# Optimization experiments

Measured on AMD Instinct MI355X. Metric: run time of the kernel, lower is better.

The kernel has to match this reference:

```python
import jax, jax.numpy as jnp
import numpy as np

B, L, H, NH = 2, 2048, 1024, 16
HD = H // NH  # head dim = 64


def setup_inputs() -> dict:
    key = jax.random.key(0)
    ks = jax.random.split(key, 8)
    s = 0.02  # small init scale for weights
    return {
        "q": jax.random.normal(ks[0], (B, L, H), jnp.float32),
        "k": jax.random.normal(ks[1], (B, L, H), jnp.float32),
        "v": jax.random.normal(ks[2], (B, L, H), jnp.float32),
        "attention_mask": jnp.zeros((B, NH, L, L), jnp.float32),
        "Wq": jax.random.normal(ks[3], (H, H), jnp.float32) * s,
        "bq": jnp.zeros((H,), jnp.float32),
        "Wk": jax.random.normal(ks[4], (H, H), jnp.float32) * s,
        "bk": jnp.zeros((H,), jnp.float32),
        "Wv": jax.random.normal(ks[5], (H, H), jnp.float32) * s,
        "bv": jnp.zeros((H,), jnp.float32),
        "Wo": jax.random.normal(ks[6], (H, H), jnp.float32) * s,
        "bo": jnp.zeros((H,), jnp.float32),
    }


def reference(q, k, v, attention_mask, Wq, bq, Wk, bk, Wv, bv, Wo, bo):
    # Conv1D (GPT-2 style) projections: x @ W + b
    query = q @ Wq + bq  # [B, L, H]
    key = k @ Wk + bk
    value = v @ Wv + bv
    # split heads -> [B, NH, L, HD]
    qh = query.reshape(B, L, NH, HD).transpose(0, 2, 1, 3)
    kh = key.reshape(B, L, NH, HD).transpose(0, 2, 1, 3)
    vh = value.reshape(B, L, NH, HD).transpose(0, 2, 1, 3)
    # scores: [B, NH, L, L]
    w = jnp.einsum("bhqd,bhkd->bhqk", qh, kh) / jnp.sqrt(jnp.float32(HD))
    w = w + attention_mask
    w = jax.nn.softmax(w, axis=-1)  # dropout p=0 -> identity
    out = jnp.einsum("bhqk,bhkd->bhqd", w, vh)  # [B, NH, L, HD]
    # merge heads -> [B, L, H]
    out = out.transpose(0, 2, 1, 3).reshape(B, L, H)
    return out @ Wo + bo
```

## Files before the change

### kernel.cpp

```cpp
#include <hip/hip_runtime.h>

#define NBATCH 2
#define LSEQ   2048
#define NH     16
#define HD     64
#define HDIM   1024
#define MTOK   4096

typedef unsigned short u16;
typedef __attribute__((ext_vector_type(8))) short bf16x8;
typedef __attribute__((ext_vector_type(4))) float f32x4;

__device__ __forceinline__ u16 f2bf(float f) {
  union { float f; unsigned int u; } x; x.f = f;
  return (u16)((x.u + 0x7fffu + ((x.u >> 16) & 1u)) >> 16);
}

__device__ __forceinline__ void gload_lds16(const void* g, void* l) {
  __builtin_amdgcn_global_load_lds(
      (const __attribute__((address_space(1))) unsigned int*)g,
      (__attribute__((address_space(3))) unsigned int*)l, 16, 0, 0);
}

__global__ void cvt3_kernel(const float* __restrict__ q, const float* __restrict__ k,
                            const float* __restrict__ v, u16* __restrict__ xq,
                            u16* __restrict__ xk, u16* __restrict__ xv) {
  const float* in;
  u16* out;
  if (blockIdx.z == 0)      { in = q; out = xq; }
  else if (blockIdx.z == 1) { in = k; out = xk; }
  else                      { in = v; out = xv; }
  int i = blockIdx.x * blockDim.x + threadIdx.x;
  float4 t = ((const float4*)in)[i];
  ushort4 o;
  o.x = f2bf(t.x); o.y = f2bf(t.y); o.z = f2bf(t.z); o.w = f2bf(t.w);
  ((ushort4*)out)[i] = o;
}

__global__ void wt4_kernel(const float* __restrict__ W0, const float* __restrict__ W1,
                           const float* __restrict__ W2, const float* __restrict__ W3,
                           u16* __restrict__ T0, u16* __restrict__ T1,
                           u16* __restrict__ T2, u16* __restrict__ T3) {
  const float* W;
  u16* Wt;
  if (blockIdx.z == 0)      { W = W0; Wt = T0; }
  else if (blockIdx.z == 1) { W = W1; Wt = T1; }
  else if (blockIdx.z == 2) { W = W2; Wt = T2; }
  else                      { W = W3; Wt = T3; }
  __shared__ float tile[64][65];
  const int k0 = (blockIdx.x & 15) << 6;
  const int n0 = (blockIdx.x >> 4) << 6;
  const int t = threadIdx.x;
#pragma unroll
  for (int i = 0; i < 4; ++i) {
    int idx = t + i * 256;
    int r = idx >> 4, c = (idx & 15) << 2;
    float4 v = *(const float4*)&W[(size_t)(k0 + r) * HDIM + n0 + c];
    tile[r][c] = v.x; tile[r][c + 1] = v.y; tile[r][c + 2] = v.z; tile[r][c + 3] = v.w;
  }
  __syncthreads();
#pragma unroll
  for (int i = 0; i < 4; ++i) {
    int idx = t + i * 256;
    int r = idx >> 4, c = (idx & 15) << 2;
    ushort4 o;
    o.x = f2bf(tile[c][r]);     o.y = f2bf(tile[c + 1][r]);
    o.z = f2bf(tile[c + 2][r]); o.w = f2bf(tile[c + 3][r]);
    *(ushort4*)&Wt[(size_t)(n0 + r) * HDIM + k0 + c] = o;
  }
}

template <int MODE>
__device__ __forceinline__ void gemm_core(u16* As, u16* Bs,
    const u16* __restrict__ A, const u16* __restrict__ Bt,
    const float* __restrict__ bias, void* __restrict__ Cout) {
  const int tid = threadIdx.x;
  const int lane = tid & 63, wid = tid >> 6;
  const int l15 = lane & 15, g = lane >> 4;
  const int m0 = blockIdx.y * 128, n0 = blockIdx.x * 128;
  const int wr = wid >> 1, wc = wid & 1;
  f32x4 acc[4][4];
#pragma unroll
  for (int i = 0; i < 4; ++i)
#pragma unroll
    for (int j = 0; j < 4; ++j) acc[i][j] = (f32x4){0.f, 0.f, 0.f, 0.f};

  for (int t = 0; t < HDIM / 64; ++t) {
    const int k0 = t * 64;
    __syncthreads();
#pragma unroll
    for (int i = 0; i < 4; ++i) {
      const int row = wid * 32 + i * 8 + (lane >> 3);
      const int colb = (lane & 7) * 16;
      gload_lds16((const char*)(A + (size_t)(m0 + row) * HDIM + k0) + colb,
                  (char*)As + (wid * 32 + i * 8) * 128);
      gload_lds16((const char*)(Bt + (size_t)(n0 + row) * HDIM + k0) + colb,
                  (char*)Bs + (wid * 32 + i * 8) * 128);
    }
    __syncthreads();
#pragma unroll
    for (int ks = 0; ks < 2; ++ks) {
      bf16x8 a[4], b[4];
#pragma unroll
      for (int i = 0; i < 4; ++i) {
        const int row = wr * 64 + i * 16 + l15;
        a[i] = *(const bf16x8*)((const char*)As + row * 128 + ks * 64 + g * 16);
      }
#pragma unroll
      for (int j = 0; j < 4; ++j) {
        const int row = wc * 64 + j * 16 + l15;
        b[j] = *(const bf16x8*)((const char*)Bs + row * 128 + ks * 64 + g * 16);
      }
#pragma unroll
      for (int i = 0; i < 4; ++i)
#pragma unroll
        for (int j = 0; j < 4; ++j)
          acc[i][j] = __builtin_amdgcn_mfma_f32_16x16x32_bf16(a[i], b[j], acc[i][j], 0, 0, 0);
    }
  }
#pragma unroll
  for (int i = 0; i < 4; ++i) {
    const int mrow = m0 + wr * 64 + i * 16 + 4 * g;
#pragma unroll
    for (int j = 0; j < 4; ++j) {
      const int ncol = n0 + wc * 64 + j * 16 + l15;
      const float bb = bias[ncol];
      if (MODE == 3) {
        float* o = (float*)Cout;
#pragma unroll
        for (int r = 0; r < 4; ++r)
          o[(size_t)(mrow + r) * HDIM + ncol] = acc[i][j][r] + bb;
      } else if (MODE == 2) {
        const int bidx = mrow >> 11, l0 = mrow & (LSEQ - 1);
        const int h = ncol >> 6, d = ncol & 63;
        ushort4 o4;
        o4.x = f2bf(acc[i][j][0] + bb); o4.y = f2bf(acc[i][j][1] + bb);
        o4.z = f2bf(acc[i][j][2] + bb); o4.w = f2bf(acc[i][j][3] + bb);
        *(ushort4*)&((u16*)Cout)[(((size_t)bidx * NH + h) * HD + d) * LSEQ + l0] = o4;
      } else {
        const int h = ncol >> 6, d = ncol & 63;
        u16* o = (u16*)Cout;
#pragma unroll
        for (int r = 0; r < 4; ++r) {
          const int m = mrow + r;
          const int bidx = m >> 11, l = m & (LSEQ - 1);
          o[(((size_t)bidx * NH + h) * LSEQ + l) * HD + d] = f2bf(acc[i][j][r] + bb);
        }
      }
    }
  }
}

__global__ __launch_bounds__(256, 2) void proj_gemm_kernel(
    const u16* __restrict__ xq, const u16* __restrict__ xk, const u16* __restrict__ xv,
    const u16* __restrict__ WqT, const u16* __restrict__ WkT, const u16* __restrict__ WvT,
    const float* __restrict__ bq, const float* __restrict__ bk, const float* __restrict__ bv,
    u16* __restrict__ Qh, u16* __restrict__ Kh, u16* __restrict__ Vt) {
  __shared__ u16 As[128 * 64];
  __shared__ u16 Bs[128 * 64];
  if (blockIdx.z == 0)      gemm_core<0>(As, Bs, xq, WqT, bq, Qh);
  else if (blockIdx.z == 1) gemm_core<0>(As, Bs, xk, WkT, bk, Kh);
  else                      gemm_core<2>(As, Bs, xv, WvT, bv, Vt);
}

__global__ __launch_bounds__(256, 2) void out_gemm_kernel(
    const u16* __restrict__ A, const u16* __restrict__ WoT,
    const float* __restrict__ bo, float* __restrict__ out) {
  __shared__ u16 As[128 * 64];
  __shared__ u16 Bs[128 * 64];
  gemm_core<3>(As, Bs, A, WoT, bo, out);
}

__global__ __launch_bounds__(256, 4) void attn_kernel(
    const u16* __restrict__ Qh, const u16* __restrict__ Kh,
    const u16* __restrict__ Vt, const float* __restrict__ mask,
    u16* __restrict__ Out ) {
  __shared__ u16 Ks[2][64 * 64];
  __shared__ u16 Vs[2][64 * 64];
  __shared__ u16 Ps[4][16 * 64];
  const int lane = threadIdx.x & 63, w = threadIdx.x >> 6;
  const int l15 = lane & 15, g = lane >> 4;
  const int bh = blockIdx.y;
  const int q0 = blockIdx.x * 64 + w * 16;

  bf16x8 aq[2];
  {
    const u16* qbase = Qh + ((size_t)bh * LSEQ + q0 + l15) * HD;
    aq[0] = *(const bf16x8*)(qbase + g * 8);
    aq[1] = *(const bf16x8*)(qbase + 32 + g * 8);
  }
  f32x4 o_acc[4];
#pragma unroll
  for (int db = 0; db < 4; ++db) o_acc[db] = (f32x4){0.f, 0.f, 0.f, 0.f};
  float m_r[4], l_r[4];
#pragma unroll
  for (int r = 0; r < 4; ++r) { m_r[r] = -1e30f; l_r[r] = 0.f; }

  const size_t kbase = (size_t)bh * LSEQ * HD;
  const size_t vbase = (size_t)bh * HD * LSEQ;
  const int srow = w * 16 + (lane >> 3);
  const int scolb = (lane & 7) * 16;

#define STAGE(buf, tt) do {                                                    \
    const int kv0_ = (tt) * 64;                                                \
    _Pragma("unroll")                                                          \
    for (int i_ = 0; i_ < 2; ++i_) {                                           \
      const int row_ = srow + i_ * 8;                                          \
      const int cb_ = scolb ^ ((row_ & 7) << 4);                               \
      gload_lds16((const char*)(Kh + kbase + (size_t)(kv0_ + row_) * HD) + cb_,\
                  (char*)Ks[buf] + (w * 16 + i_ * 8) * 128);                   \
      gload_lds16((const char*)(Vt + vbase + (size_t)row_ * LSEQ + kv0_) + cb_,\
                  (char*)Vs[buf] + (w * 16 + i_ * 8) * 128);                   \
    }                                                                          \
  } while (0)

  STAGE(0, 0);
  __syncthreads();

  int cur = 0;
  const float* mbase0 = mask + ((size_t)bh * LSEQ + q0 + 4 * g) * LSEQ + l15;
  u16* pbase = Ps[w];

  for (int t = 0; t < LSEQ / 64; ++t) {
    const int kv0 = t * 64;
    if (t + 1 < LSEQ / 64) STAGE(cur ^ 1, t + 1);

    float mv[4][4];
#pragma unroll
    for (int r = 0; r < 4; ++r)
#pragma unroll
      for (int nb = 0; nb < 4; ++nb)
        mv[r][nb] = mbase0[(size_t)r * LSEQ + kv0 + nb * 16];

    f32x4 s_acc[4];
#pragma unroll
    for (int nb = 0; nb < 4; ++nb) s_acc[nb] = (f32x4){0.f, 0.f, 0.f, 0.f};
#pragma unroll
    for (int ks = 0; ks < 2; ++ks) {
#pragma unroll
      for (int nb = 0; nb < 4; ++nb) {
        const int row = nb * 16 + l15;
        bf16x8 bk = *(const bf16x8*)((const char*)Ks[cur] + row * 128 +
                                     ((ks * 64 + g * 16) ^ ((row & 7) << 4)));
        s_acc[nb] = __builtin_amdgcn_mfma_f32_16x16x32_bf16(aq[ks], bk, s_acc[nb], 0, 0, 0);
      }
    }

#pragma unroll
    for (int r = 0; r < 4; ++r) {
      float v0 = s_acc[0][r] * 0.125f + mv[r][0];
      float v1 = s_acc[1][r] * 0.125f + mv[r][1];
      float v2 = s_acc[2][r] * 0.125f + mv[r][2];
      float v3 = s_acc[3][r] * 0.125f + mv[r][3];
      float mm = fmaxf(fmaxf(v0, v1), fmaxf(v2, v3));
      mm = fmaxf(mm, __shfl_xor(mm, 1));
      mm = fmaxf(mm, __shfl_xor(mm, 2));
      mm = fmaxf(mm, __shfl_xor(mm, 4));
      mm = fmaxf(mm, __shfl_xor(mm, 8));
      const float mnew = fmaxf(m_r[r], mm);
      const float cf = __expf(m_r[r] - mnew);
      m_r[r] = mnew;
      float p0 = __expf(v0 - mnew), p1 = __expf(v1 - mnew);
      float p2 = __expf(v2 - mnew), p3 = __expf(v3 - mnew);
      float s0 = p0 + p1 + p2 + p3;
      s0 += __shfl_xor(s0, 1); s0 += __shfl_xor(s0, 2);
      s0 += __shfl_xor(s0, 4); s0 += __shfl_xor(s0, 8);
      l_r[r] = l_r[r] * cf + s0;
#pragma unroll
      for (int db = 0; db < 4; ++db) o_acc[db][r] *= cf;
      const int q = 4 * g + r;
      const int qx = (q & 7) << 4;
      *(u16*)((char*)pbase + q * 128 + ((0 + 2 * l15) ^ qx)) = f2bf(p0);
      *(u16*)((char*)pbase + q * 128 + ((32 + 2 * l15) ^ qx)) = f2bf(p1);
      *(u16*)((char*)pbase + q * 128 + ((64 + 2 * l15) ^ qx)) = f2bf(p2);
      *(u16*)((char*)pbase + q * 128 + ((96 + 2 * l15) ^ qx)) = f2bf(p3);
    }
    asm volatile("s_waitcnt lgkmcnt(0)" ::: "memory");
    __builtin_amdgcn_sched_barrier(0);

#pragma unroll
    for (int s = 0; s < 2; ++s) {
      bf16x8 pa = *(const bf16x8*)((const char*)pbase + l15 * 128 +
                                   ((s * 64 + 16 * g) ^ ((l15 & 7) << 4)));
#pragma unroll
      for (int db = 0; db < 4; ++db) {
        const int row = db * 16 + l15;
        bf16x8 bv = *(const bf16x8*)((const char*)Vs[cur] + row * 128 +
                                     ((s * 64 + 16 * g) ^ ((row & 7) << 4)));
        o_acc[db] = __builtin_amdgcn_mfma_f32_16x16x32_bf16(pa, bv, o_acc[db], 0, 0, 0);
      }
    }
    __syncthreads();
    cur ^= 1;
  }
#undef STAGE

  const int b = bh >> 4, h = bh & 15;
#pragma unroll
  for (int r = 0; r < 4; ++r) {
    const float inv = 1.f / l_r[r];
    const int qg = q0 + 4 * g + r;
    u16* orow = Out + ((size_t)(b * LSEQ + qg) * NH + h) * HD;
#pragma unroll
    for (int db = 0; db < 4; ++db)
      orow[db * 16 + l15] = f2bf(o_acc[db][r] * inv);
  }
}

extern "C" void kernel_launch(void* const* d_in, const int* in_sizes, int n_in,
                              void* d_out, int out_size, void* d_ws, size_t ws_size,
                              hipStream_t stream) {
  (void)in_sizes; (void)n_in; (void)out_size; (void)ws_size;
  const float* q    = (const float*)d_in[0];
  const float* k    = (const float*)d_in[1];
  const float* v    = (const float*)d_in[2];
  const float* mask = (const float*)d_in[3];
  const float* Wq   = (const float*)d_in[4];
  const float* bq   = (const float*)d_in[5];
  const float* Wk   = (const float*)d_in[6];
  const float* bk   = (const float*)d_in[7];
  const float* Wv   = (const float*)d_in[8];
  const float* bv   = (const float*)d_in[9];
  const float* Wo   = (const float*)d_in[10];
  const float* bo   = (const float*)d_in[11];
  float* out = (float*)d_out;

  char* ws = (char*)d_ws;
  const size_t XB = (size_t)MTOK * HDIM * 2;
  const size_t WB = (size_t)HDIM * HDIM * 2;
  u16* xq   = (u16*)(ws);
  u16* xk   = (u16*)(ws + XB);
  u16* xv   = (u16*)(ws + 2 * XB);
  u16* WqT  = (u16*)(ws + 3 * XB);
  u16* WkT  = (u16*)(ws + 3 * XB + WB);
  u16* WvT  = (u16*)(ws + 3 * XB + 2 * WB);
  u16* WoT  = (u16*)(ws + 3 * XB + 3 * WB);
  u16* Qh   = (u16*)(ws + 3 * XB + 4 * WB);
  u16* Kh   = (u16*)(ws + 4 * XB + 4 * WB);
  u16* Vt   = (u16*)(ws + 5 * XB + 4 * WB);
  u16* aout = (u16*)(ws + 6 * XB + 4 * WB);

  cvt3_kernel<<<dim3((MTOK * HDIM) / 4 / 256, 1, 3), 256, 0, stream>>>(
      q, k, v, xq, xk, xv);
  wt4_kernel<<<dim3(256, 1, 4), 256, 0, stream>>>(
      Wq, Wk, Wv, Wo, WqT, WkT, WvT, WoT);
  proj_gemm_kernel<<<dim3(HDIM / 128, MTOK / 128, 3), 256, 0, stream>>>(
      xq, xk, xv, WqT, WkT, WvT, bq, bk, bv, Qh, Kh, Vt);
  attn_kernel<<<dim3(LSEQ / 64, NBATCH * NH), 256, 0, stream>>>(Qh, Kh, Vt, mask, aout);
  out_gemm_kernel<<<dim3(HDIM / 128, MTOK / 128), 256, 0, stream>>>(aout, WoT, bo, out);
}
```

Before: 246.2 us.

## Transpose QK^T MFMA so each lane owns one query row for softmax

Swaps the MFMA operands for the score computation so each lane holds four scores from a single query row. Softmax max and sum then reduce across only two cross-lane shuffles instead of four per row, and the running max and sum live in one scalar per lane. Mask values are loaded as float4 and prefetched one tile ahead, P is written to LDS as packed 4-element stores, and s_setprio raises wave priority around the MFMA blocks. The cost is extra shuffles to spread rescale factors and row sums back to the output accumulator layout.

```diff
diff --git a/kernel.cpp b/kernel.cpp
--- a/kernel.cpp
+++ b/kernel.cpp
@@ -182,6 +182,7 @@
   const int l15 = lane & 15, g = lane >> 4;
   const int bh = blockIdx.y;
   const int q0 = blockIdx.x * 64 + w * 16;
+  const int NT = LSEQ / 64;
 
   bf16x8 aq[2];
   {
@@ -192,9 +193,7 @@
   f32x4 o_acc[4];
 #pragma unroll
   for (int db = 0; db < 4; ++db) o_acc[db] = (f32x4){0.f, 0.f, 0.f, 0.f};
-  float m_r[4], l_r[4];
-#pragma unroll
-  for (int r = 0; r < 4; ++r) { m_r[r] = -1e30f; l_r[r] = 0.f; }
+  float m_run = -1e30f, l_run = 0.f;
 
   const size_t kbase = (size_t)bh * LSEQ * HD;
   const size_t vbase = (size_t)bh * HD * LSEQ;
@@ -214,74 +213,96 @@
     }                                                                          \
   } while (0)
 
+  const float* mrow = mask + ((size_t)bh * LSEQ + q0 + l15) * LSEQ;
+  f32x4 mv[4];
+
   STAGE(0, 0);
+#pragma unroll
+  for (int mb = 0; mb < 4; ++mb)
+    mv[mb] = *(const f32x4*)(mrow + mb * 16 + 4 * g);
   __syncthreads();
 
   int cur = 0;
-  const float* mbase0 = mask + ((size_t)bh * LSEQ + q0 + 4 * g) * LSEQ + l15;
   u16* pbase = Ps[w];
-
-  for (int t = 0; t < LSEQ / 64; ++t) {
-    const int kv0 = t * 64;
-    if (t + 1 < LSEQ / 64) STAGE(cur ^ 1, t + 1);
-
-    float mv[4][4];
-#pragma unroll
-    for (int r = 0; r < 4; ++r)
-#pragma unroll
-      for (int nb = 0; nb < 4; ++nb)
-        mv[r][nb] = mbase0[(size_t)r * LSEQ + kv0 + nb * 16];
+  const int srcbase = (lane & 48) | ((lane & 48) >> 2);
+  const int pswz = (l15 & 7) << 4;
+
+  for (int t = 0; t < NT; ++t) {
+    if (t + 1 < NT) STAGE(cur ^ 1, t + 1);
 
     f32x4 s_acc[4];
 #pragma unroll
-    for (int nb = 0; nb < 4; ++nb) s_acc[nb] = (f32x4){0.f, 0.f, 0.f, 0.f};
+    for (int mb = 0; mb < 4; ++mb) s_acc[mb] = (f32x4){0.f, 0.f, 0.f, 0.f};
+    __builtin_amdgcn_s_setprio(1);
 #pragma unroll
     for (int ks = 0; ks < 2; ++ks) {
 #pragma unroll
-      for (int nb = 0; nb < 4; ++nb) {
-        const int row = nb * 16 + l15;
+      for (int mb = 0; mb < 4; ++mb) {
+        const int row = mb * 16 + l15;
         bf16x8 bk = *(const bf16x8*)((const char*)Ks[cur] + row * 128 +
                                      ((ks * 64 + g * 16) ^ ((row & 7) << 4)));
-        s_acc[nb] = __builtin_amdgcn_mfma_f32_16x16x32_bf16(aq[ks], bk, s_acc[nb], 0, 0, 0);
-      }
-    }
-
-#pragma unroll
-    for (int r = 0; r < 4; ++r) {
-      float v0 = s_acc[0][r] * 0.125f + mv[r][0];
-      float v1 = s_acc[1][r] * 0.125f + mv[r][1];
-      float v2 = s_acc[2][r] * 0.125f + mv[r][2];
-      float v3 = s_acc[3][r] * 0.125f + mv[r][3];
-      float mm = fmaxf(fmaxf(v0, v1), fmaxf(v2, v3));
-      mm = fmaxf(mm, __shfl_xor(mm, 1));
-      mm = fmaxf(mm, __shfl_xor(mm, 2));
-      mm = fmaxf(mm, __shfl_xor(mm, 4));
-      mm = fmaxf(mm, __shfl_xor(mm, 8));
-      const float mnew = fmaxf(m_r[r], mm);
-      const float cf = __expf(m_r[r] - mnew);
-      m_r[r] = mnew;
-      float p0 = __expf(v0 - mnew), p1 = __expf(v1 - mnew);
-      float p2 = __expf(v2 - mnew), p3 = __expf(v3 - mnew);
-      float s0 = p0 + p1 + p2 + p3;
-      s0 += __shfl_xor(s0, 1); s0 += __shfl_xor(s0, 2);
-      s0 += __shfl_xor(s0, 4); s0 += __shfl_xor(s0, 8);
-      l_r[r] = l_r[r] * cf + s0;
-#pragma unroll
-      for (int db = 0; db < 4; ++db) o_acc[db][r] *= cf;
-      const int q = 4 * g + r;
-      const int qx = (q & 7) << 4;
-      *(u16*)((char*)pbase + q * 128 + ((0 + 2 * l15) ^ qx)) = f2bf(p0);
-      *(u16*)((char*)pbase + q * 128 + ((32 + 2 * l15) ^ qx)) = f2bf(p1);
-      *(u16*)((char*)pbase + q * 128 + ((64 + 2 * l15) ^ qx)) = f2bf(p2);
-      *(u16*)((char*)pbase + q * 128 + ((96 + 2 * l15) ^ qx)) = f2bf(p3);
-    }
+        s_acc[mb] = __builtin_amdgcn_mfma_f32_16x16x32_bf16(bk, aq[ks], s_acc[mb], 0, 0, 0);
+      }
+    }
+    __builtin_amdgcn_s_setprio(0);
+
+    float p[4][4];
+    float tmax = -1e30f;
+#pragma unroll
+    for (int mb = 0; mb < 4; ++mb)
+#pragma unroll
+      for (int r = 0; r < 4; ++r) {
+        p[mb][r] = s_acc[mb][r] * 0.125f + mv[mb][r];
+        tmax = fmaxf(tmax, p[mb][r]);
+      }
+    tmax = fmaxf(tmax, __shfl_xor(tmax, 16));
+    tmax = fmaxf(tmax, __shfl_xor(tmax, 32));
+    const float mnew = fmaxf(m_run, tmax);
+    const float cf = __expf(m_run - mnew);
+    m_run = mnew;
+    float psum = 0.f;
+#pragma unroll
+    for (int mb = 0; mb < 4; ++mb)
+#pragma unroll
+      for (int r = 0; r < 4; ++r) {
+        p[mb][r] = __expf(p[mb][r] - mnew);
+        psum += p[mb][r];
+      }
+    psum += __shfl_xor(psum, 16);
+    psum += __shfl_xor(psum, 32);
+    l_run = l_run * cf + psum;
+    float cfr[4];
+#pragma unroll
+    for (int r = 0; r < 4; ++r) cfr[r] = __shfl(cf, srcbase + r);
+#pragma unroll
+    for (int db = 0; db < 4; ++db)
+#pragma unroll
+      for (int r = 0; r < 4; ++r) o_acc[db][r] *= cfr[r];
+
+#pragma unroll
+    for (int mb = 0; mb < 4; ++mb) {
+      ushort4 pk;
+      pk.x = f2bf(p[mb][0]); pk.y = f2bf(p[mb][1]);
+      pk.z = f2bf(p[mb][2]); pk.w = f2bf(p[mb][3]);
+      *(ushort4*)((char*)pbase + l15 * 128 + ((mb * 32 + 8 * g) ^ pswz)) = pk;
+    }
+
+    {
+      const int tn = (t + 1 < NT) ? t + 1 : t;
+      const float* mnext = mrow + tn * 64;
+#pragma unroll
+      for (int mb = 0; mb < 4; ++mb)
+        mv[mb] = *(const f32x4*)(mnext + mb * 16 + 4 * g);
+    }
+
     asm volatile("s_waitcnt lgkmcnt(0)" ::: "memory");
     __builtin_amdgcn_sched_barrier(0);
 
+    __builtin_amdgcn_s_setprio(1);
 #pragma unroll
     for (int s = 0; s < 2; ++s) {
       bf16x8 pa = *(const bf16x8*)((const char*)pbase + l15 * 128 +
-                                   ((s * 64 + 16 * g) ^ ((l15 & 7) << 4)));
+                                   ((s * 64 + 16 * g) ^ pswz));
 #pragma unroll
       for (int db = 0; db < 4; ++db) {
         const int row = db * 16 + l15;
@@ -290,15 +311,19 @@
         o_acc[db] = __builtin_amdgcn_mfma_f32_16x16x32_bf16(pa, bv, o_acc[db], 0, 0, 0);
       }
     }
+    __builtin_amdgcn_s_setprio(0);
     __syncthreads();
     cur ^= 1;
   }
 #undef STAGE
 
   const int b = bh >> 4, h = bh & 15;
+  float lr[4];
+#pragma unroll
+  for (int r = 0; r < 4; ++r) lr[r] = __shfl(l_run, srcbase + r);
 #pragma unroll
   for (int r = 0; r < 4; ++r) {
-    const float inv = 1.f / l_r[r];
+    const float inv = 1.f / lr[r];
     const int qg = q0 + 4 * g + r;
     u16* orow = Out + ((size_t)(b * LSEQ + qg) * NH + h) * HD;
 #pragma unroll
```

New measurement: 232.8 us. -5.4%, faster.

## Transpose S layout, lazy softmax rescale, prefetch mask two tiles ahead

Applied to the files above, without the earlier changes.

Swaps the MFMA operands for QK^T so each lane holds one query row's scores. The row max and sum then need only two cross-lane shuffles instead of four per row. The online-softmax rescale of the output accumulator is skipped unless some row's max grows by more than 8, which trades some fp32 headroom for fewer exp and multiply operations. Mask values are loaded as vectorized f32x4 two tiles ahead into double registers, the KV loop is unrolled by two with setprio around the MFMA blocks, and the syncthreads is replaced by a vmcnt-limited wait plus s_barrier.

```diff
diff --git a/kernel.cpp b/kernel.cpp
--- a/kernel.cpp
+++ b/kernel.cpp
@@ -182,6 +182,7 @@
   const int l15 = lane & 15, g = lane >> 4;
   const int bh = blockIdx.y;
   const int q0 = blockIdx.x * 64 + w * 16;
+  const int NT = LSEQ / 64;
 
   bf16x8 aq[2];
   {
@@ -192,9 +193,7 @@
   f32x4 o_acc[4];
 #pragma unroll
   for (int db = 0; db < 4; ++db) o_acc[db] = (f32x4){0.f, 0.f, 0.f, 0.f};
-  float m_r[4], l_r[4];
-#pragma unroll
-  for (int r = 0; r < 4; ++r) { m_r[r] = -1e30f; l_r[r] = 0.f; }
+  float m_run = -1e30f, l_run = 0.f;
 
   const size_t kbase = (size_t)bh * LSEQ * HD;
   const size_t vbase = (size_t)bh * HD * LSEQ;
@@ -214,91 +213,132 @@
     }                                                                          \
   } while (0)
 
+  const float* mrow = mask + ((size_t)bh * LSEQ + q0 + l15) * LSEQ;
+  f32x4 mvA[4], mvB[4];
+
   STAGE(0, 0);
+#pragma unroll
+  for (int mb = 0; mb < 4; ++mb) {
+    mvA[mb] = *(const f32x4*)(mrow + 0 * 64 + mb * 16 + 4 * g);
+    mvB[mb] = *(const f32x4*)(mrow + 1 * 64 + mb * 16 + 4 * g);
+  }
   __syncthreads();
 
-  int cur = 0;
-  const float* mbase0 = mask + ((size_t)bh * LSEQ + q0 + 4 * g) * LSEQ + l15;
   u16* pbase = Ps[w];
-
-  for (int t = 0; t < LSEQ / 64; ++t) {
-    const int kv0 = t * 64;
-    if (t + 1 < LSEQ / 64) STAGE(cur ^ 1, t + 1);
-
-    float mv[4][4];
-#pragma unroll
-    for (int r = 0; r < 4; ++r)
-#pragma unroll
-      for (int nb = 0; nb < 4; ++nb)
-        mv[r][nb] = mbase0[(size_t)r * LSEQ + kv0 + nb * 16];
-
-    f32x4 s_acc[4];
-#pragma unroll
-    for (int nb = 0; nb < 4; ++nb) s_acc[nb] = (f32x4){0.f, 0.f, 0.f, 0.f};
-#pragma unroll
-    for (int ks = 0; ks < 2; ++ks) {
-#pragma unroll
-      for (int nb = 0; nb < 4; ++nb) {
-        const int row = nb * 16 + l15;
-        bf16x8 bk = *(const bf16x8*)((const char*)Ks[cur] + row * 128 +
-                                     ((ks * 64 + g * 16) ^ ((row & 7) << 4)));
-        s_acc[nb] = __builtin_amdgcn_mfma_f32_16x16x32_bf16(aq[ks], bk, s_acc[nb], 0, 0, 0);
-      }
-    }
-
-#pragma unroll
-    for (int r = 0; r < 4; ++r) {
-      float v0 = s_acc[0][r] * 0.125f + mv[r][0];
-      float v1 = s_acc[1][r] * 0.125f + mv[r][1];
-      float v2 = s_acc[2][r] * 0.125f + mv[r][2];
-      float v3 = s_acc[3][r] * 0.125f + mv[r][3];
-      float mm = fmaxf(fmaxf(v0, v1), fmaxf(v2, v3));
-      mm = fmaxf(mm, __shfl_xor(mm, 1));
-      mm = fmaxf(mm, __shfl_xor(mm, 2));
-      mm = fmaxf(mm, __shfl_xor(mm, 4));
-      mm = fmaxf(mm, __shfl_xor(mm, 8));
-      const float mnew = fmaxf(m_r[r], mm);
-      const float cf = __expf(m_r[r] - mnew);
-      m_r[r] = mnew;
-      float p0 = __expf(v0 - mnew), p1 = __expf(v1 - mnew);
-      float p2 = __expf(v2 - mnew), p3 = __expf(v3 - mnew);
-      float s0 = p0 + p1 + p2 + p3;
-      s0 += __shfl_xor(s0, 1); s0 += __shfl_xor(s0, 2);
-      s0 += __shfl_xor(s0, 4); s0 += __shfl_xor(s0, 8);
-      l_r[r] = l_r[r] * cf + s0;
-#pragma unroll
-      for (int db = 0; db < 4; ++db) o_acc[db][r] *= cf;
-      const int q = 4 * g + r;
-      const int qx = (q & 7) << 4;
-      *(u16*)((char*)pbase + q * 128 + ((0 + 2 * l15) ^ qx)) = f2bf(p0);
-      *(u16*)((char*)pbase + q * 128 + ((32 + 2 * l15) ^ qx)) = f2bf(p1);
-      *(u16*)((char*)pbase + q * 128 + ((64 + 2 * l15) ^ qx)) = f2bf(p2);
-      *(u16*)((char*)pbase + q * 128 + ((96 + 2 * l15) ^ qx)) = f2bf(p3);
-    }
-    asm volatile("s_waitcnt lgkmcnt(0)" ::: "memory");
-    __builtin_amdgcn_sched_barrier(0);
-
-#pragma unroll
-    for (int s = 0; s < 2; ++s) {
-      bf16x8 pa = *(const bf16x8*)((const char*)pbase + l15 * 128 +
-                                   ((s * 64 + 16 * g) ^ ((l15 & 7) << 4)));
-#pragma unroll
-      for (int db = 0; db < 4; ++db) {
-        const int row = db * 16 + l15;
-        bf16x8 bv = *(const bf16x8*)((const char*)Vs[cur] + row * 128 +
-                                     ((s * 64 + 16 * g) ^ ((row & 7) << 4)));
-        o_acc[db] = __builtin_amdgcn_mfma_f32_16x16x32_bf16(pa, bv, o_acc[db], 0, 0, 0);
-      }
-    }
-    __syncthreads();
-    cur ^= 1;
-  }
+  const int srcbase = (lane & 48) | ((lane & 48) >> 2);
+  const int pswz = (l15 & 7) << 4;
+
+#define TILE_BODY(t, cur, mv) do {                                            \
+    if ((t) + 1 < NT) STAGE((cur) ^ 1, (t) + 1);                              \
+               \
+    f32x4 s_acc[4];                                                           \
+    _Pragma("unroll")                                                         \
+    for (int mb = 0; mb < 4; ++mb) s_acc[mb] = (f32x4){0.f, 0.f, 0.f, 0.f};   \
+    __builtin_amdgcn_s_setprio(1);                                            \
+    _Pragma("unroll")                                                         \
+    for (int ks = 0; ks < 2; ++ks) {                                          \
+      _Pragma("unroll")                                                       \
+      for (int mb = 0; mb < 4; ++mb) {                                        \
+        const int row = mb * 16 + l15;                                        \
+        bf16x8 bk = *(const bf16x8*)((const char*)Ks[cur] + row * 128 +       \
+                                     ((ks * 64 + g * 16) ^ ((row & 7) << 4)));\
+        s_acc[mb] = __builtin_amdgcn_mfma_f32_16x16x32_bf16(bk, aq[ks],       \
+                                                            s_acc[mb], 0,0,0);\
+      }                                                                       \
+    }                                                                         \
+    __builtin_amdgcn_s_setprio(0);                                            \
+                              \
+    float p[4][4];                                                            \
+    float tmax = -1e30f;                                                      \
+    _Pragma("unroll")                                                         \
+    for (int mb = 0; mb < 4; ++mb)                                            \
+      _Pragma("unroll")                                                       \
+      for (int r = 0; r < 4; ++r) {                                           \
+        p[mb][r] = s_acc[mb][r] * 0.125f + mv[mb][r];                         \
+        tmax = fmaxf(tmax, p[mb][r]);                                         \
+      }                                                                       \
+    tmax = fmaxf(tmax, __shfl_xor(tmax, 16));                                 \
+    tmax = fmaxf(tmax, __shfl_xor(tmax, 32));                                 \
+    if (!__all(tmax - m_run <= 8.f)) {                     \
+      const float mnew = fmaxf(m_run, tmax);                                  \
+      const float cf = __expf(m_run - mnew);                                  \
+      m_run = mnew;                                                           \
+      l_run *= cf;                                                            \
+      float cfr[4];                                                           \
+      _Pragma("unroll")                                                       \
+      for (int r = 0; r < 4; ++r) cfr[r] = __shfl(cf, srcbase + r);           \
+      _Pragma("unroll")                                                       \
+      for (int db = 0; db < 4; ++db)                                          \
+        _Pragma("unroll")                                                     \
+        for (int r = 0; r < 4; ++r) o_acc[db][r] *= cfr[r];                   \
+    }                                                                         \
+    float psum = 0.f;                                                         \
+    _Pragma("unroll")                                                         \
+    for (int mb = 0; mb < 4; ++mb)                                            \
+      _Pragma("unroll")                                                       \
+      for (int r = 0; r < 4; ++r) {                                           \
+        p[mb][r] = __expf(p[mb][r] - m_run);                                  \
+        psum += p[mb][r];                                                     \
+      }                                                                       \
+    psum += __shfl_xor(psum, 16);                                             \
+    psum += __shfl_xor(psum, 32);                                             \
+    l_run += psum;                                                            \
+                             \
+    _Pragma("unroll")                                                         \
+    for (int mb = 0; mb < 4; ++mb) {                                          \
+      ushort4 pk;                                                             \
+      pk.x = f2bf(p[mb][0]); pk.y = f2bf(p[mb][1]);                           \
+      pk.z = f2bf(p[mb][2]); pk.w = f2bf(p[mb][3]);                           \
+      *(ushort4*)((char*)pbase + l15 * 128 + ((mb * 32 + 8 * g) ^ pswz)) = pk;\
+    }                                                                         \
+           \
+    __builtin_amdgcn_sched_barrier(0);                                        \
+    {                                                                         \
+      const int tn = ((t) + 2 < NT) ? (t) + 2 : NT - 1;                       \
+      const float* mnext = mrow + tn * 64;                                    \
+      _Pragma("unroll")                                                       \
+      for (int mb = 0; mb < 4; ++mb)                                          \
+        mv[mb] = *(const f32x4*)(mnext + mb * 16 + 4 * g);                    \
+    }                                                                         \
+                      \
+    asm volatile("s_waitcnt lgkmcnt(0)" ::: "memory");                        \
+    __builtin_amdgcn_sched_barrier(0);                                        \
+                                                                \
+    __builtin_amdgcn_s_setprio(1);                                            \
+    _Pragma("unroll")                                                         \
+    for (int s = 0; s < 2; ++s) {                                             \
+      bf16x8 pa = *(const bf16x8*)((const char*)pbase + l15 * 128 +           \
+                                   ((s * 64 + 16 * g) ^ pswz));               \
+      _Pragma("unroll")                                                       \
+      for (int db = 0; db < 4; ++db) {                                        \
+        const int row = db * 16 + l15;                                        \
+        bf16x8 bv = *(const bf16x8*)((const char*)Vs[cur] + row * 128 +       \
+                                     ((s * 64 + 16 * g) ^ ((row & 7) << 4))); \
+        o_acc[db] = __builtin_amdgcn_mfma_f32_16x16x32_bf16(pa, bv,           \
+                                                            o_acc[db], 0,0,0);\
+      }                                                                       \
+    }                                                                         \
+    __builtin_amdgcn_s_setprio(0);                                            \
+         \
+    asm volatile("s_waitcnt vmcnt(4)" ::: "memory");                          \
+    __builtin_amdgcn_s_barrier();                                             \
+    __builtin_amdgcn_sched_barrier(0);                                        \
+  } while (0)
+
+  for (int t = 0; t < NT; t += 2) {
+    TILE_BODY(t, 0, mvA);
+    TILE_BODY(t + 1, 1, mvB);
+  }
+#undef TILE_BODY
 #undef STAGE
 
   const int b = bh >> 4, h = bh & 15;
+  float lr[4];
+#pragma unroll
+  for (int r = 0; r < 4; ++r) lr[r] = __shfl(l_run, srcbase + r);
 #pragma unroll
   for (int r = 0; r < 4; ++r) {
-    const float inv = 1.f / l_r[r];
+    const float inv = 1.f / lr[r];
     const int qg = q0 + 4 * g + r;
     u16* orow = Out + ((size_t)(b * LSEQ + qg) * NH + h) * HD;
 #pragma unroll
```

Measured after the change: 233.4 us. -5.2%, faster.
